# Kernel optimization log

Measured on AMD Instinct MI355X. Metric: run time of the kernel, lower is better.

Reference implementation:

```python
import jax, jax.numpy as jnp
import numpy as np

B, N, M, NF = 8, 512, 100, 42
DIMS = [NF, 256, 128, 64, 1]


def setup_inputs() -> dict:
    key = jax.random.key(0)
    ks = jax.random.split(key, 3 + len(DIMS) - 1)
    inp = {
        "image": jax.random.normal(ks[0], (B, N, NF), jnp.float32),
        "dfeat": jax.random.normal(ks[1], (B, N, M, NF, 3), jnp.float32) * 0.1,
        "neighbor": jax.random.randint(ks[2], (B, N, M), 0, N + 1),  # 0 = no neighbor, else 1-based atom idx
    }
    for l in range(len(DIMS) - 1):
        inp[f"W{l}"] = jax.random.normal(ks[3 + l], (DIMS[l], DIMS[l + 1]), jnp.float32) / np.sqrt(DIMS[l])
        inp[f"b{l}"] = jnp.zeros((DIMS[l + 1],), jnp.float32)
    return inp


def _atom_energy(x, Ws, bs):
    # per-atom MLP: sigmoid hidden layers, linear scalar output
    h = x
    for W, b in zip(Ws[:-1], bs[:-1]):
        h = jax.nn.sigmoid(h @ W + b)
    return (h @ Ws[-1] + bs[-1])[0]


def reference(image, dfeat, neighbor, W0, b0, W1, b1, W2, b2, W3, b3):
    Ws = (W0, W1, W2, W3)
    bs = (b0, b1, b2, b3)
    nb, na, nf = image.shape

    e_fn = lambda x: _atom_energy(x, Ws, bs)
    flat = image.reshape(-1, nf)
    Ei = jax.vmap(e_fn)(flat).reshape(nb, na)                      # [B, N]
    dE = jax.vmap(jax.grad(e_fn))(flat).reshape(nb, na, nf)        # dEi/dFeat, [B, N, F]
    Etot = jnp.sum(Ei, axis=1, keepdims=True)                      # [B, 1]

    # Force[b,i,:] = sum_m dE[b, neighbor[b,i,m]-1, :] @ dfeat[b,i,m,:,:], masking pad (0) entries
    mask = (neighbor > 0).astype(dE.dtype)                         # [B, N, M]
    idx = jnp.maximum(neighbor - 1, 0)                             # [B, N, M]
    dE_g = jax.vmap(lambda d, i: d[i])(dE, idx)                    # [B, N, M, F]
    Force = jnp.einsum('bnmf,bnmfd->bnd', dE_g * mask[..., None], dfeat)  # [B, N, 3]
    return Etot, Ei, Force
```

## Files before the change

kernel.cpp:

```cpp
#include <hip/hip_runtime.h>

#define NFEAT 42
#define H1 256
#define H2 128
#define H3 64
#define NB 8
#define NA 512
#define NM 100
#define TA 4

__device__ __forceinline__ float sigmoidf(float z) {
    return 1.0f / (1.0f + __expf(-z));
}

__global__ __launch_bounds__(256) void transpose_weights(
    const float* __restrict__ W0, const float* __restrict__ W1, const float* __restrict__ W2,
    float* __restrict__ W0T, float* __restrict__ W1T, float* __restrict__ W2T)
{
    int i = blockIdx.x * 256 + threadIdx.x;
    if (i < H1 * NFEAT) {
        int k = i / NFEAT, f = i - k * NFEAT;
        W0T[i] = W0[f * H1 + k];
    }
    if (i < H2 * H1) {
        int j = i >> 8, k = i & 255;
        W1T[i] = W1[k * H2 + j];
    }
    if (i < H3 * H2) {
        int k = i >> 7, j = i & 127;
        W2T[i] = W2[j * H3 + k];
    }
}

__global__ __launch_bounds__(256) void mlp_fwd_bwd(
    const float* __restrict__ image,
    const float* __restrict__ W0, const float* __restrict__ b0,
    const float* __restrict__ W1, const float* __restrict__ b1,
    const float* __restrict__ W2, const float* __restrict__ b2,
    const float* __restrict__ W3, const float* __restrict__ b3,
    const float* __restrict__ W0T, const float* __restrict__ W1T, const float* __restrict__ W2T,
    float* __restrict__ Ei,
    float* __restrict__ dE)
{
    const int t = threadIdx.x;
    const int atom0 = blockIdx.x * TA;

    __shared__ __align__(16) float sx[TA][NFEAT + 2];
    __shared__ __align__(16) float sh1[TA][H1];
    __shared__ __align__(16) float sh2[TA][H2];
    __shared__ __align__(16) float sh3[TA][H3];
    __shared__ __align__(16) float sd3[TA][H3];
    __shared__ __align__(16) float sd2[TA][H2];
    __shared__ __align__(16) float sd1[TA][H1];

    for (int i = t; i < TA * NFEAT; i += 256) {
        int a = i / NFEAT, f = i - a * NFEAT;
        sx[a][f] = image[(atom0 + a) * NFEAT + f];
    }
    __syncthreads();

    {
        float acc[TA] = {0.f, 0.f, 0.f, 0.f};
        for (int kk = 0; kk < 10; ++kk) {
            float w0_ = W0[(4 * kk + 0) * H1 + t];
            float w1_ = W0[(4 * kk + 1) * H1 + t];
            float w2_ = W0[(4 * kk + 2) * H1 + t];
            float w3_ = W0[(4 * kk + 3) * H1 + t];
            #pragma unroll
            for (int a = 0; a < TA; ++a) {
                float4 h = ((const float4*)sx[a])[kk];
                acc[a] += h.x * w0_ + h.y * w1_ + h.z * w2_ + h.w * w3_;
            }
        }
        float wa = W0[40 * H1 + t], wb = W0[41 * H1 + t];
        float bb = b0[t];
        #pragma unroll
        for (int a = 0; a < TA; ++a) {
            acc[a] += sx[a][40] * wa + sx[a][41] * wb;
            sh1[a][t] = sigmoidf(acc[a] + bb);
        }
    }
    __syncthreads();

    {
        const int j = t & 127, a0 = (t >> 7) * 2;
        float acc[2] = {0.f, 0.f};
        for (int kk = 0; kk < H1 / 4; ++kk) {
            float w0_ = W1[(4 * kk + 0) * H2 + j];
            float w1_ = W1[(4 * kk + 1) * H2 + j];
            float w2_ = W1[(4 * kk + 2) * H2 + j];
            float w3_ = W1[(4 * kk + 3) * H2 + j];
            #pragma unroll
            for (int a = 0; a < 2; ++a) {
                float4 h = ((const float4*)sh1[a0 + a])[kk];
                acc[a] += h.x * w0_ + h.y * w1_ + h.z * w2_ + h.w * w3_;
            }
        }
        float bb = b1[j];
        #pragma unroll
        for (int a = 0; a < 2; ++a) sh2[a0 + a][j] = sigmoidf(acc[a] + bb);
    }
    __syncthreads();

    {
        const int j = t & 63, a = t >> 6;
        float acc = 0.f;
        for (int kk = 0; kk < H2 / 4; ++kk) {
            float w0_ = W2[(4 * kk + 0) * H3 + j];
            float w1_ = W2[(4 * kk + 1) * H3 + j];
            float w2_ = W2[(4 * kk + 2) * H3 + j];
            float w3_ = W2[(4 * kk + 3) * H3 + j];
            float4 h = ((const float4*)sh2[a])[kk];
            acc += h.x * w0_ + h.y * w1_ + h.z * w2_ + h.w * w3_;
        }
        sh3[a][j] = sigmoidf(acc + b2[j]);
    }
    __syncthreads();

    {
        const int lane = t & 63, a = t >> 6;
        float w = W3[lane];
        float h = sh3[a][lane];
        sd3[a][lane] = w * h * (1.f - h);
        float v = w * h;
        #pragma unroll
        for (int off = 32; off > 0; off >>= 1) v += __shfl_down(v, off, 64);
        if (lane == 0) Ei[atom0 + a] = v + b3[0];
    }
    __syncthreads();

    {
        const int j = t & 127, a0 = (t >> 7) * 2;
        float acc[2] = {0.f, 0.f};
        for (int kk = 0; kk < H3 / 4; ++kk) {
            float w0_ = W2T[(4 * kk + 0) * H2 + j];
            float w1_ = W2T[(4 * kk + 1) * H2 + j];
            float w2_ = W2T[(4 * kk + 2) * H2 + j];
            float w3_ = W2T[(4 * kk + 3) * H2 + j];
            #pragma unroll
            for (int a = 0; a < 2; ++a) {
                float4 d = ((const float4*)sd3[a0 + a])[kk];
                acc[a] += d.x * w0_ + d.y * w1_ + d.z * w2_ + d.w * w3_;
            }
        }
        #pragma unroll
        for (int a = 0; a < 2; ++a) {
            float h = sh2[a0 + a][j];
            sd2[a0 + a][j] = acc[a] * h * (1.f - h);
        }
    }
    __syncthreads();

    {
        float acc[TA] = {0.f, 0.f, 0.f, 0.f};
        for (int jj = 0; jj < H2 / 4; ++jj) {
            float w0_ = W1T[(4 * jj + 0) * H1 + t];
            float w1_ = W1T[(4 * jj + 1) * H1 + t];
            float w2_ = W1T[(4 * jj + 2) * H1 + t];
            float w3_ = W1T[(4 * jj + 3) * H1 + t];
            #pragma unroll
            for (int a = 0; a < TA; ++a) {
                float4 d = ((const float4*)sd2[a])[jj];
                acc[a] += d.x * w0_ + d.y * w1_ + d.z * w2_ + d.w * w3_;
            }
        }
        #pragma unroll
        for (int a = 0; a < TA; ++a) {
            float h = sh1[a][t];
            sd1[a][t] = acc[a] * h * (1.f - h);
        }
    }
    __syncthreads();

    {
        const int f = t & 63, a = t >> 6;
        if (f < NFEAT) {
            float acc = 0.f;
            for (int kk = 0; kk < H1 / 4; ++kk) {
                float w0_ = W0T[(4 * kk + 0) * NFEAT + f];
                float w1_ = W0T[(4 * kk + 1) * NFEAT + f];
                float w2_ = W0T[(4 * kk + 2) * NFEAT + f];
                float w3_ = W0T[(4 * kk + 3) * NFEAT + f];
                float4 d = ((const float4*)sd1[a])[kk];
                acc += d.x * w0_ + d.y * w1_ + d.z * w2_ + d.w * w3_;
            }
            dE[(atom0 + a) * NFEAT + f] = acc;
        }
    }
}

__global__ __launch_bounds__(256) void etot_kernel(const float* __restrict__ Ei,
                                                   float* __restrict__ Etot)
{
    const int b = blockIdx.x;
    const int t = threadIdx.x;
    float v = Ei[b * NA + t] + Ei[b * NA + t + 256];
    __shared__ float red[4];
    #pragma unroll
    for (int off = 32; off > 0; off >>= 1) v += __shfl_down(v, off, 64);
    if ((t & 63) == 0) red[t >> 6] = v;
    __syncthreads();
    if (t == 0) Etot[b] = red[0] + red[1] + red[2] + red[3];
}

__global__ __launch_bounds__(256) void force_kernel(
    const float* __restrict__ dfeat,
    const int*   __restrict__ neighbor,
    const float* __restrict__ dE,
    float* __restrict__ Force)
{
    const int bi = blockIdx.x;
    const int b  = bi >> 9;
    const int t  = threadIdx.x;

    __shared__ int   s_nb[NM];
    __shared__ float s_dE[104 * NFEAT];
    __shared__ float s_part[1008];
    __shared__ float s_red[126];

    if (t < NM) s_nb[t] = neighbor[bi * NM + t];
    for (int i = t; i < 4 * NFEAT; i += 256) s_dE[NM * NFEAT + i] = 0.f;
    __syncthreads();

    for (int i = t; i < NM * NFEAT; i += 256) {
        int m = i / NFEAT, f = i - m * NFEAT;
        int n = s_nb[m];
        s_dE[i] = (n > 0) ? dE[((b << 9) + n - 1) * NFEAT + f] : 0.f;
    }
    __syncthreads();

    if (t < 252) {
        const int e4 = 4 * t;
        int off[4];
        #pragma unroll
        for (int c = 0; c < 4; ++c) {
            int ee = e4 + c;
            int r  = ee / 126;
            int e  = ee - r * 126;
            off[c] = r * NFEAT + e / 3;
        }
        const float* base = dfeat + (size_t)bi * (NM * NFEAT * 3);
        float acc[4] = {0.f, 0.f, 0.f, 0.f};

        for (int m0 = 0; m0 < 48; m0 += 8) {
            float4 vA = *(const float4*)(base + m0 * 126 + e4);
            float4 vB = *(const float4*)(base + (m0 + 48) * 126 + e4);
            const float* sdA = s_dE + m0 * NFEAT;
            const float* sdB = s_dE + (m0 + 48) * NFEAT;
            acc[0] += vA.x * sdA[off[0]] + vB.x * sdB[off[0]];
            acc[1] += vA.y * sdA[off[1]] + vB.y * sdB[off[1]];
            acc[2] += vA.z * sdA[off[2]] + vB.z * sdB[off[2]];
            acc[3] += vA.w * sdA[off[3]] + vB.w * sdB[off[3]];
        }
        {
            const int m0 = 96;
            float vv[4];
            if (bi != NB * NA - 1) {
                float4 v = *(const float4*)(base + m0 * 126 + e4);
                vv[0] = v.x; vv[1] = v.y; vv[2] = v.z; vv[3] = v.w;
            } else {
                #pragma unroll
                for (int c = 0; c < 4; ++c) {
                    int r = (e4 + c) / 126;
                    vv[c] = (m0 + r < NM) ? base[m0 * 126 + e4 + c] : 0.f;
                }
            }
            const float* sd = s_dE + m0 * NFEAT;
            #pragma unroll
            for (int c = 0; c < 4; ++c) acc[c] += vv[c] * sd[off[c]];
        }
        #pragma unroll
        for (int c = 0; c < 4; ++c) s_part[e4 + c] = acc[c];
    }
    __syncthreads();

    if (t < 126) {
        float s = 0.f;
        #pragma unroll
        for (int r = 0; r < 8; ++r) s += s_part[r * 126 + t];
        s_red[t] = s;
    }
    __syncthreads();

    if (t < 3) {
        float s = 0.f;
        #pragma unroll
        for (int f = 0; f < NFEAT; ++f) s += s_red[f * 3 + t];
        Force[bi * 3 + t] = s;
    }
}

extern "C" void kernel_launch(void* const* d_in, const int* in_sizes, int n_in,
                              void* d_out, int out_size, void* d_ws, size_t ws_size,
                              hipStream_t stream) {
    const float* image    = (const float*)d_in[0];
    const float* dfeat    = (const float*)d_in[1];
    const int*   neighbor = (const int*)  d_in[2];
    const float* W0 = (const float*)d_in[3];
    const float* b0 = (const float*)d_in[4];
    const float* W1 = (const float*)d_in[5];
    const float* b1 = (const float*)d_in[6];
    const float* W2 = (const float*)d_in[7];
    const float* b2 = (const float*)d_in[8];
    const float* W3 = (const float*)d_in[9];
    const float* b3 = (const float*)d_in[10];

    float* out   = (float*)d_out;
    float* Etot  = out;
    float* Ei    = out + NB;
    float* Force = out + NB + NB * NA;

    float* dE  = (float*)d_ws;
    float* W0T = dE  + NB * NA * NFEAT;
    float* W1T = W0T + H1 * NFEAT;
    float* W2T = W1T + H2 * H1;

    transpose_weights<<<(H1 * H2 + 255) / 256, 256, 0, stream>>>(W0, W1, W2, W0T, W1T, W2T);
    mlp_fwd_bwd<<<(NB * NA) / TA, 256, 0, stream>>>(image, W0, b0, W1, b1, W2, b2, W3, b3,
                                                    W0T, W1T, W2T, Ei, dE);
    etot_kernel<<<NB, 256, 0, stream>>>(Ei, Etot);
    force_kernel<<<NB * NA, 256, 0, stream>>>(dfeat, neighbor, dE, Force);
}
```

Baseline: 346.6 us.

## Stage MLP weights through shared memory and double atoms per block

```diff
diff --git a/kernel.cpp b/kernel.cpp
--- a/kernel.cpp
+++ b/kernel.cpp
@@ -7,7 +7,7 @@
 #define NB 8
 #define NA 512
 #define NM 100
-#define TA 4
+#define TA 8
 
 __device__ __forceinline__ float sigmoidf(float z) {
     return 1.0f / (1.0f + __expf(-z));
@@ -52,27 +52,52 @@
     __shared__ __align__(16) float sd3[TA][H3];
     __shared__ __align__(16) float sd2[TA][H2];
     __shared__ __align__(16) float sd1[TA][H1];
+    __shared__ __align__(16) float wbuf[6144];
+
+    auto stage = [&](const float* src, int nf) {
+        __syncthreads();
+        const float4* s4 = (const float4*)src;
+        float4* d4 = (float4*)wbuf;
+        int n4 = nf >> 2;
+        for (int i = t; i < n4; i += 256) d4[i] = s4[i];
+        __syncthreads();
+    };
 
     for (int i = t; i < TA * NFEAT; i += 256) {
         int a = i / NFEAT, f = i - a * NFEAT;
         sx[a][f] = image[(atom0 + a) * NFEAT + f];
     }
-    __syncthreads();
-
-    {
-        float acc[TA] = {0.f, 0.f, 0.f, 0.f};
-        for (int kk = 0; kk < 10; ++kk) {
-            float w0_ = W0[(4 * kk + 0) * H1 + t];
-            float w1_ = W0[(4 * kk + 1) * H1 + t];
-            float w2_ = W0[(4 * kk + 2) * H1 + t];
-            float w3_ = W0[(4 * kk + 3) * H1 + t];
+
+    {
+        float acc[TA];
+        #pragma unroll
+        for (int a = 0; a < TA; ++a) acc[a] = 0.f;
+
+        stage(W0, 24 * H1);
+        for (int kq = 0; kq < 6; ++kq) {
+            float w0_ = wbuf[(4 * kq + 0) * H1 + t];
+            float w1_ = wbuf[(4 * kq + 1) * H1 + t];
+            float w2_ = wbuf[(4 * kq + 2) * H1 + t];
+            float w3_ = wbuf[(4 * kq + 3) * H1 + t];
             #pragma unroll
             for (int a = 0; a < TA; ++a) {
-                float4 h = ((const float4*)sx[a])[kk];
+                float4 h = ((const float4*)sx[a])[kq];
                 acc[a] += h.x * w0_ + h.y * w1_ + h.z * w2_ + h.w * w3_;
             }
         }
-        float wa = W0[40 * H1 + t], wb = W0[41 * H1 + t];
+        stage(W0 + 24 * H1, 18 * H1);
+        for (int kq = 0; kq < 4; ++kq) {
+            float w0_ = wbuf[(4 * kq + 0) * H1 + t];
+            float w1_ = wbuf[(4 * kq + 1) * H1 + t];
+            float w2_ = wbuf[(4 * kq + 2) * H1 + t];
+            float w3_ = wbuf[(4 * kq + 3) * H1 + t];
+            #pragma unroll
+            for (int a = 0; a < TA; ++a) {
+                float4 h = ((const float4*)sx[a])[6 + kq];
+                acc[a] += h.x * w0_ + h.y * w1_ + h.z * w2_ + h.w * w3_;
+            }
+        }
+        float wa = wbuf[16 * H1 + t], wb = wbuf[17 * H1 + t];
         float bb = b0[t];
         #pragma unroll
         for (int a = 0; a < TA; ++a) {
@@ -80,88 +105,119 @@
             sh1[a][t] = sigmoidf(acc[a] + bb);
         }
     }
-    __syncthreads();
-
-    {
-        const int j = t & 127, a0 = (t >> 7) * 2;
+
+    {
+        const int j = t & 127, a0 = (t >> 7) * 4;
+        float acc[4] = {0.f, 0.f, 0.f, 0.f};
+        for (int c = 0; c < 6; ++c) {
+            const int k0 = 48 * c;
+            const int nrow = (c < 5) ? 48 : 16;
+            stage(W1 + k0 * H2, nrow * H2);
+            const int q0 = k0 >> 2;
+            for (int kq = 0; kq < nrow / 4; ++kq) {
+                float w0_ = wbuf[(4 * kq + 0) * H2 + j];
+                float w1_ = wbuf[(4 * kq + 1) * H2 + j];
+                float w2_ = wbuf[(4 * kq + 2) * H2 + j];
+                float w3_ = wbuf[(4 * kq + 3) * H2 + j];
+                #pragma unroll
+                for (int a = 0; a < 4; ++a) {
+                    float4 h = ((const float4*)sh1[a0 + a])[q0 + kq];
+                    acc[a] += h.x * w0_ + h.y * w1_ + h.z * w2_ + h.w * w3_;
+                }
+            }
+        }
+        float bb = b1[j];
+        #pragma unroll
+        for (int a = 0; a < 4; ++a) sh2[a0 + a][j] = sigmoidf(acc[a] + bb);
+    }
+
+    {
+        const int j = t & 63, a0 = (t >> 6) * 2;
         float acc[2] = {0.f, 0.f};
-        for (int kk = 0; kk < H1 / 4; ++kk) {
-            float w0_ = W1[(4 * kk + 0) * H2 + j];
-            float w1_ = W1[(4 * kk + 1) * H2 + j];
-            float w2_ = W1[(4 * kk + 2) * H2 + j];
-            float w3_ = W1[(4 * kk + 3) * H2 + j];
-            #pragma unroll
-            for (int a = 0; a < 2; ++a) {
-                float4 h = ((const float4*)sh1[a0 + a])[kk];
-                acc[a] += h.x * w0_ + h.y * w1_ + h.z * w2_ + h.w * w3_;
-            }
-        }
-        float bb = b1[j];
-        #pragma unroll
-        for (int a = 0; a < 2; ++a) sh2[a0 + a][j] = sigmoidf(acc[a] + bb);
-    }
-    __syncthreads();
-
-    {
-        const int j = t & 63, a = t >> 6;
-        float acc = 0.f;
-        for (int kk = 0; kk < H2 / 4; ++kk) {
-            float w0_ = W2[(4 * kk + 0) * H3 + j];
-            float w1_ = W2[(4 * kk + 1) * H3 + j];
-            float w2_ = W2[(4 * kk + 2) * H3 + j];
-            float w3_ = W2[(4 * kk + 3) * H3 + j];
-            float4 h = ((const float4*)sh2[a])[kk];
-            acc += h.x * w0_ + h.y * w1_ + h.z * w2_ + h.w * w3_;
-        }
-        sh3[a][j] = sigmoidf(acc + b2[j]);
-    }
-    __syncthreads();
-
-    {
-        const int lane = t & 63, a = t >> 6;
+        for (int c = 0; c < 2; ++c) {
+            const int k0 = (c == 0) ? 0 : 96;
+            const int nrow = (c == 0) ? 96 : 32;
+            stage(W2 + k0 * H3, nrow * H3);
+            const int q0 = k0 >> 2;
+            for (int kq = 0; kq < nrow / 4; ++kq) {
+                float w0_ = wbuf[(4 * kq + 0) * H3 + j];
+                float w1_ = wbuf[(4 * kq + 1) * H3 + j];
+                float w2_ = wbuf[(4 * kq + 2) * H3 + j];
+                float w3_ = wbuf[(4 * kq + 3) * H3 + j];
+                #pragma unroll
+                for (int a = 0; a < 2; ++a) {
+                    float4 h = ((const float4*)sh2[a0 + a])[q0 + kq];
+                    acc[a] += h.x * w0_ + h.y * w1_ + h.z * w2_ + h.w * w3_;
+                }
+            }
+        }
+        float bb = b2[j];
+        #pragma unroll
+        for (int a = 0; a < 2; ++a) sh3[a0 + a][j] = sigmoidf(acc[a] + bb);
+    }
+    __syncthreads();
+
+    {
+        const int lane = t & 63, a0 = (t >> 6) * 2;
         float w = W3[lane];
-        float h = sh3[a][lane];
-        sd3[a][lane] = w * h * (1.f - h);
-        float v = w * h;
-        #pragma unroll
-        for (int off = 32; off > 0; off >>= 1) v += __shfl_down(v, off, 64);
-        if (lane == 0) Ei[atom0 + a] = v + b3[0];
-    }
-    __syncthreads();
-
-    {
-        const int j = t & 127, a0 = (t >> 7) * 2;
-        float acc[2] = {0.f, 0.f};
-        for (int kk = 0; kk < H3 / 4; ++kk) {
-            float w0_ = W2T[(4 * kk + 0) * H2 + j];
-            float w1_ = W2T[(4 * kk + 1) * H2 + j];
-            float w2_ = W2T[(4 * kk + 2) * H2 + j];
-            float w3_ = W2T[(4 * kk + 3) * H2 + j];
-            #pragma unroll
-            for (int a = 0; a < 2; ++a) {
-                float4 d = ((const float4*)sd3[a0 + a])[kk];
-                acc[a] += d.x * w0_ + d.y * w1_ + d.z * w2_ + d.w * w3_;
-            }
-        }
-        #pragma unroll
-        for (int a = 0; a < 2; ++a) {
+        float bb = b3[0];
+        #pragma unroll
+        for (int a = a0; a < a0 + 2; ++a) {
+            float h = sh3[a][lane];
+            sd3[a][lane] = w * h * (1.f - h);
+            float v = w * h;
+            #pragma unroll
+            for (int off = 32; off > 0; off >>= 1) v += __shfl_down(v, off, 64);
+            if (lane == 0) Ei[atom0 + a] = v + bb;
+        }
+    }
+
+    {
+        const int j = t & 127, a0 = (t >> 7) * 4;
+        float acc[4] = {0.f, 0.f, 0.f, 0.f};
+        for (int c = 0; c < 2; ++c) {
+            const int k0 = (c == 0) ? 0 : 48;
+            const int nrow = (c == 0) ? 48 : 16;
+            stage(W2T + k0 * H2, nrow * H2);
+            const int q0 = k0 >> 2;
+            for (int kq = 0; kq < nrow / 4; ++kq) {
+                float w0_ = wbuf[(4 * kq + 0) * H2 + j];
+                float w1_ = wbuf[(4 * kq + 1) * H2 + j];
+                float w2_ = wbuf[(4 * kq + 2) * H2 + j];
+                float w3_ = wbuf[(4 * kq + 3) * H2 + j];
+                #pragma unroll
+                for (int a = 0; a < 4; ++a) {
+                    float4 d = ((const float4*)sd3[a0 + a])[q0 + kq];
+                    acc[a] += d.x * w0_ + d.y * w1_ + d.z * w2_ + d.w * w3_;
+                }
+            }
+        }
+        #pragma unroll
+        for (int a = 0; a < 4; ++a) {
             float h = sh2[a0 + a][j];
             sd2[a0 + a][j] = acc[a] * h * (1.f - h);
         }
     }
-    __syncthreads();
-
-    {
-        float acc[TA] = {0.f, 0.f, 0.f, 0.f};
-        for (int jj = 0; jj < H2 / 4; ++jj) {
-            float w0_ = W1T[(4 * jj + 0) * H1 + t];
-            float w1_ = W1T[(4 * jj + 1) * H1 + t];
-            float w2_ = W1T[(4 * jj + 2) * H1 + t];
-            float w3_ = W1T[(4 * jj + 3) * H1 + t];
-            #pragma unroll
-            for (int a = 0; a < TA; ++a) {
-                float4 d = ((const float4*)sd2[a])[jj];
-                acc[a] += d.x * w0_ + d.y * w1_ + d.z * w2_ + d.w * w3_;
+
+    {
+        float acc[TA];
+        #pragma unroll
+        for (int a = 0; a < TA; ++a) acc[a] = 0.f;
+        for (int c = 0; c < 6; ++c) {
+            const int j0 = 24 * c;
+            const int nrow = (c < 5) ? 24 : 8;
+            stage(W1T + j0 * H1, nrow * H1);
+            const int q0 = j0 >> 2;
+            for (int jq = 0; jq < nrow / 4; ++jq) {
+                float w0_ = wbuf[(4 * jq + 0) * H1 + t];
+                float w1_ = wbuf[(4 * jq + 1) * H1 + t];
+                float w2_ = wbuf[(4 * jq + 2) * H1 + t];
+                float w3_ = wbuf[(4 * jq + 3) * H1 + t];
+                #pragma unroll
+                for (int a = 0; a < TA; ++a) {
+                    float4 d = ((const float4*)sd2[a])[q0 + jq];
+                    acc[a] += d.x * w0_ + d.y * w1_ + d.z * w2_ + d.w * w3_;
+                }
             }
         }
         #pragma unroll
@@ -170,21 +226,33 @@
             sd1[a][t] = acc[a] * h * (1.f - h);
         }
     }
-    __syncthreads();
-
-    {
-        const int f = t & 63, a = t >> 6;
+
+    {
+        const int f = t & 63, a0 = (t >> 6) * 2;
+        float acc[2] = {0.f, 0.f};
+        for (int c = 0; c < 2; ++c) {
+            const int k0 = (c == 0) ? 0 : 144;
+            const int nrow = (c == 0) ? 144 : 112;
+            stage(W0T + k0 * NFEAT, nrow * NFEAT);
+            if (f < NFEAT) {
+                const int q0 = k0 >> 2;
+                for (int kq = 0; kq < nrow / 4; ++kq) {
+                    float w0_ = wbuf[(4 * kq + 0) * NFEAT + f];
+                    float w1_ = wbuf[(4 * kq + 1) * NFEAT + f];
+                    float w2_ = wbuf[(4 * kq + 2) * NFEAT + f];
+                    float w3_ = wbuf[(4 * kq + 3) * NFEAT + f];
+                    #pragma unroll
+                    for (int a = 0; a < 2; ++a) {
+                        float4 d = ((const float4*)sd1[a0 + a])[q0 + kq];
+                        acc[a] += d.x * w0_ + d.y * w1_ + d.z * w2_ + d.w * w3_;
+                    }
+                }
+            }
+        }
         if (f < NFEAT) {
-            float acc = 0.f;
-            for (int kk = 0; kk < H1 / 4; ++kk) {
-                float w0_ = W0T[(4 * kk + 0) * NFEAT + f];
-                float w1_ = W0T[(4 * kk + 1) * NFEAT + f];
-                float w2_ = W0T[(4 * kk + 2) * NFEAT + f];
-                float w3_ = W0T[(4 * kk + 3) * NFEAT + f];
-                float4 d = ((const float4*)sd1[a])[kk];
-                acc += d.x * w0_ + d.y * w1_ + d.z * w2_ + d.w * w3_;
-            }
-            dE[(atom0 + a) * NFEAT + f] = acc;
+            #pragma unroll
+            for (int a = 0; a < 2; ++a)
+                dE[(atom0 + a0 + a) * NFEAT + f] = acc[a];
         }
     }
 }
```

After: 638.9 us. 84.3% more time.

## Split fused per-atom MLP into layer-wise kernels with transposed activation layout

Applied to the files above, without the earlier changes.

```diff
diff --git a/kernel.cpp b/kernel.cpp
--- a/kernel.cpp
+++ b/kernel.cpp
@@ -7,10 +7,29 @@
 #define NB 8
 #define NA 512
 #define NM 100
-#define TA 4
+#define NTOT (NB * NA)
 
 __device__ __forceinline__ float sigmoidf(float z) {
     return 1.0f / (1.0f + __expf(-z));
+}
+
+template<int K, int JT>
+__device__ __forceinline__ void mv(const float* __restrict__ actT,
+                                   const float* __restrict__ WT,
+                                   int j0, int n, float* __restrict__ acc) {
+    static_assert(K % 64 == 0, "K must be a multiple of 64");
+    #pragma unroll
+    for (int c = 0; c < K / 64; ++c) {
+        float act[64];
+        #pragma unroll
+        for (int i = 0; i < 64; ++i) act[i] = actT[(c * 64 + i) * NTOT + n];
+        #pragma unroll
+        for (int j = 0; j < JT; ++j) {
+            const float* w = WT + (j0 + j) * K + c * 64;
+            #pragma unroll
+            for (int i = 0; i < 64; ++i) acc[j] += act[i] * w[i];
+        }
+    }
 }
 
 __global__ __launch_bounds__(256) void transpose_weights(
@@ -19,8 +38,8 @@
 {
     int i = blockIdx.x * 256 + threadIdx.x;
     if (i < H1 * NFEAT) {
-        int k = i / NFEAT, f = i - k * NFEAT;
-        W0T[i] = W0[f * H1 + k];
+        int j = i / NFEAT, f = i - j * NFEAT;
+        W0T[i] = W0[f * H1 + j];
     }
     if (i < H2 * H1) {
         int j = i >> 8, k = i & 255;
@@ -32,161 +51,125 @@
     }
 }
 
-__global__ __launch_bounds__(256) void mlp_fwd_bwd(
-    const float* __restrict__ image,
-    const float* __restrict__ W0, const float* __restrict__ b0,
-    const float* __restrict__ W1, const float* __restrict__ b1,
-    const float* __restrict__ W2, const float* __restrict__ b2,
-    const float* __restrict__ W3, const float* __restrict__ b3,
-    const float* __restrict__ W0T, const float* __restrict__ W1T, const float* __restrict__ W2T,
-    float* __restrict__ Ei,
+__global__ __launch_bounds__(256) void l0_fwd(
+    const float* __restrict__ image, const float* __restrict__ W0T,
+    const float* __restrict__ b0, float* __restrict__ h1T)
+{
+    const int t = threadIdx.x;
+    const int n0 = blockIdx.x * 256;
+    const int j0 = blockIdx.y * 8;
+
+    __shared__ float sx[256 * 43];
+    for (int i = t; i < 256 * NFEAT; i += 256) {
+        int n = i / NFEAT, f = i - n * NFEAT;
+        sx[n * 43 + f] = image[n0 * NFEAT + i];
+    }
+    __syncthreads();
+
+    float act[NFEAT];
+    #pragma unroll
+    for (int f = 0; f < NFEAT; ++f) act[f] = sx[t * 43 + f];
+
+    float acc[8];
+    #pragma unroll
+    for (int j = 0; j < 8; ++j) acc[j] = b0[j0 + j];
+    #pragma unroll
+    for (int j = 0; j < 8; ++j) {
+        const float* w = W0T + (j0 + j) * NFEAT;
+        #pragma unroll
+        for (int f = 0; f < NFEAT; ++f) acc[j] += act[f] * w[f];
+    }
+    const int n = n0 + t;
+    #pragma unroll
+    for (int j = 0; j < 8; ++j) h1T[(j0 + j) * NTOT + n] = sigmoidf(acc[j]);
+}
+
+__global__ __launch_bounds__(256) void l1_fwd(
+    const float* __restrict__ h1T, const float* __restrict__ W1T,
+    const float* __restrict__ b1, float* __restrict__ h2T)
+{
+    const int n = blockIdx.x * 256 + threadIdx.x;
+    const int j0 = blockIdx.y * 8;
+    float acc[8];
+    #pragma unroll
+    for (int j = 0; j < 8; ++j) acc[j] = b1[j0 + j];
+    mv<H1, 8>(h1T, W1T, j0, n, acc);
+    #pragma unroll
+    for (int j = 0; j < 8; ++j) h2T[(j0 + j) * NTOT + n] = sigmoidf(acc[j]);
+}
+
+__global__ __launch_bounds__(256) void l2_fwd(
+    const float* __restrict__ h2T, const float* __restrict__ W2T,
+    const float* __restrict__ b2, float* __restrict__ h3T)
+{
+    const int n = blockIdx.x * 256 + threadIdx.x;
+    const int j0 = blockIdx.y * 4;
+    float acc[4];
+    #pragma unroll
+    for (int j = 0; j < 4; ++j) acc[j] = b2[j0 + j];
+    mv<H2, 4>(h2T, W2T, j0, n, acc);
+    #pragma unroll
+    for (int j = 0; j < 4; ++j) h3T[(j0 + j) * NTOT + n] = sigmoidf(acc[j]);
+}
+
+__global__ __launch_bounds__(256) void l3_ei(
+    const float* __restrict__ h3T, const float* __restrict__ W3,
+    const float* __restrict__ b3, float* __restrict__ Ei, float* __restrict__ d3T)
+{
+    const int n = blockIdx.x * 256 + threadIdx.x;
+    float e = b3[0];
+    #pragma unroll
+    for (int k = 0; k < H3; ++k) {
+        float w = W3[k];
+        float h = h3T[k * NTOT + n];
+        e += w * h;
+        d3T[k * NTOT + n] = w * h * (1.f - h);
+    }
+    Ei[n] = e;
+}
+
+__global__ __launch_bounds__(256) void bwd_d2(
+    const float* __restrict__ d3T, const float* __restrict__ W2,
+    const float* __restrict__ h2T, float* __restrict__ d2T)
+{
+    const int n = blockIdx.x * 256 + threadIdx.x;
+    const int j0 = blockIdx.y * 4;
+    float acc[4] = {0.f, 0.f, 0.f, 0.f};
+    mv<H3, 4>(d3T, W2, j0, n, acc);
+    #pragma unroll
+    for (int j = 0; j < 4; ++j) {
+        float h = h2T[(j0 + j) * NTOT + n];
+        d2T[(j0 + j) * NTOT + n] = acc[j] * h * (1.f - h);
+    }
+}
+
+__global__ __launch_bounds__(256) void bwd_d1(
+    const float* __restrict__ d2T, const float* __restrict__ W1,
+    const float* __restrict__ h1T, float* __restrict__ d1T)
+{
+    const int n = blockIdx.x * 256 + threadIdx.x;
+    const int j0 = blockIdx.y * 8;
+    float acc[8] = {0.f, 0.f, 0.f, 0.f, 0.f, 0.f, 0.f, 0.f};
+    mv<H2, 8>(d2T, W1, j0, n, acc);
+    #pragma unroll
+    for (int j = 0; j < 8; ++j) {
+        float h = h1T[(j0 + j) * NTOT + n];
+        d1T[(j0 + j) * NTOT + n] = acc[j] * h * (1.f - h);
+    }
+}
+
+__global__ __launch_bounds__(256) void bwd_dE(
+    const float* __restrict__ d1T, const float* __restrict__ W0,
     float* __restrict__ dE)
 {
-    const int t = threadIdx.x;
-    const int atom0 = blockIdx.x * TA;
-
-    __shared__ __align__(16) float sx[TA][NFEAT + 2];
-    __shared__ __align__(16) float sh1[TA][H1];
-    __shared__ __align__(16) float sh2[TA][H2];
-    __shared__ __align__(16) float sh3[TA][H3];
-    __shared__ __align__(16) float sd3[TA][H3];
-    __shared__ __align__(16) float sd2[TA][H2];
-    __shared__ __align__(16) float sd1[TA][H1];
-
-    for (int i = t; i < TA * NFEAT; i += 256) {
-        int a = i / NFEAT, f = i - a * NFEAT;
-        sx[a][f] = image[(atom0 + a) * NFEAT + f];
-    }
-    __syncthreads();
-
-    {
-        float acc[TA] = {0.f, 0.f, 0.f, 0.f};
-        for (int kk = 0; kk < 10; ++kk) {
-            float w0_ = W0[(4 * kk + 0) * H1 + t];
-            float w1_ = W0[(4 * kk + 1) * H1 + t];
-            float w2_ = W0[(4 * kk + 2) * H1 + t];
-            float w3_ = W0[(4 * kk + 3) * H1 + t];
-            #pragma unroll
-            for (int a = 0; a < TA; ++a) {
-                float4 h = ((const float4*)sx[a])[kk];
-                acc[a] += h.x * w0_ + h.y * w1_ + h.z * w2_ + h.w * w3_;
-            }
-        }
-        float wa = W0[40 * H1 + t], wb = W0[41 * H1 + t];
-        float bb = b0[t];
-        #pragma unroll
-        for (int a = 0; a < TA; ++a) {
-            acc[a] += sx[a][40] * wa + sx[a][41] * wb;
-            sh1[a][t] = sigmoidf(acc[a] + bb);
-        }
-    }
-    __syncthreads();
-
-    {
-        const int j = t & 127, a0 = (t >> 7) * 2;
-        float acc[2] = {0.f, 0.f};
-        for (int kk = 0; kk < H1 / 4; ++kk) {
-            float w0_ = W1[(4 * kk + 0) * H2 + j];
-            float w1_ = W1[(4 * kk + 1) * H2 + j];
-            float w2_ = W1[(4 * kk + 2) * H2 + j];
-            float w3_ = W1[(4 * kk + 3) * H2 + j];
-            #pragma unroll
-            for (int a = 0; a < 2; ++a) {
-                float4 h = ((const float4*)sh1[a0 + a])[kk];
-                acc[a] += h.x * w0_ + h.y * w1_ + h.z * w2_ + h.w * w3_;
-            }
-        }
-        float bb = b1[j];
-        #pragma unroll
-        for (int a = 0; a < 2; ++a) sh2[a0 + a][j] = sigmoidf(acc[a] + bb);
-    }
-    __syncthreads();
-
-    {
-        const int j = t & 63, a = t >> 6;
-        float acc = 0.f;
-        for (int kk = 0; kk < H2 / 4; ++kk) {
-            float w0_ = W2[(4 * kk + 0) * H3 + j];
-            float w1_ = W2[(4 * kk + 1) * H3 + j];
-            float w2_ = W2[(4 * kk + 2) * H3 + j];
-            float w3_ = W2[(4 * kk + 3) * H3 + j];
-            float4 h = ((const float4*)sh2[a])[kk];
-            acc += h.x * w0_ + h.y * w1_ + h.z * w2_ + h.w * w3_;
-        }
-        sh3[a][j] = sigmoidf(acc + b2[j]);
-    }
-    __syncthreads();
-
-    {
-        const int lane = t & 63, a = t >> 6;
-        float w = W3[lane];
-        float h = sh3[a][lane];
-        sd3[a][lane] = w * h * (1.f - h);
-        float v = w * h;
-        #pragma unroll
-        for (int off = 32; off > 0; off >>= 1) v += __shfl_down(v, off, 64);
-        if (lane == 0) Ei[atom0 + a] = v + b3[0];
-    }
-    __syncthreads();
-
-    {
-        const int j = t & 127, a0 = (t >> 7) * 2;
-        float acc[2] = {0.f, 0.f};
-        for (int kk = 0; kk < H3 / 4; ++kk) {
-            float w0_ = W2T[(4 * kk + 0) * H2 + j];
-            float w1_ = W2T[(4 * kk + 1) * H2 + j];
-            float w2_ = W2T[(4 * kk + 2) * H2 + j];
-            float w3_ = W2T[(4 * kk + 3) * H2 + j];
-            #pragma unroll
-            for (int a = 0; a < 2; ++a) {
-                float4 d = ((const float4*)sd3[a0 + a])[kk];
-                acc[a] += d.x * w0_ + d.y * w1_ + d.z * w2_ + d.w * w3_;
-            }
-        }
-        #pragma unroll
-        for (int a = 0; a < 2; ++a) {
-            float h = sh2[a0 + a][j];
-            sd2[a0 + a][j] = acc[a] * h * (1.f - h);
-        }
-    }
-    __syncthreads();
-
-    {
-        float acc[TA] = {0.f, 0.f, 0.f, 0.f};
-        for (int jj = 0; jj < H2 / 4; ++jj) {
-            float w0_ = W1T[(4 * jj + 0) * H1 + t];
-            float w1_ = W1T[(4 * jj + 1) * H1 + t];
-            float w2_ = W1T[(4 * jj + 2) * H1 + t];
-            float w3_ = W1T[(4 * jj + 3) * H1 + t];
-            #pragma unroll
-            for (int a = 0; a < TA; ++a) {
-                float4 d = ((const float4*)sd2[a])[jj];
-                acc[a] += d.x * w0_ + d.y * w1_ + d.z * w2_ + d.w * w3_;
-            }
-        }
-        #pragma unroll
-        for (int a = 0; a < TA; ++a) {
-            float h = sh1[a][t];
-            sd1[a][t] = acc[a] * h * (1.f - h);
-        }
-    }
-    __syncthreads();
-
-    {
-        const int f = t & 63, a = t >> 6;
-        if (f < NFEAT) {
-            float acc = 0.f;
-            for (int kk = 0; kk < H1 / 4; ++kk) {
-                float w0_ = W0T[(4 * kk + 0) * NFEAT + f];
-                float w1_ = W0T[(4 * kk + 1) * NFEAT + f];
-                float w2_ = W0T[(4 * kk + 2) * NFEAT + f];
-                float w3_ = W0T[(4 * kk + 3) * NFEAT + f];
-                float4 d = ((const float4*)sd1[a])[kk];
-                acc += d.x * w0_ + d.y * w1_ + d.z * w2_ + d.w * w3_;
-            }
-            dE[(atom0 + a) * NFEAT + f] = acc;
-        }
-    }
+    const int n = blockIdx.x * 256 + threadIdx.x;
+    const int f0 = blockIdx.y * 14;
+    float acc[14];
+    #pragma unroll
+    for (int j = 0; j < 14; ++j) acc[j] = 0.f;
+    mv<H1, 14>(d1T, W0, f0, n, acc);
+    #pragma unroll
+    for (int j = 0; j < 14; ++j) dE[n * NFEAT + f0 + j] = acc[j];
 }
 
 __global__ __launch_bounds__(256) void etot_kernel(const float* __restrict__ Ei,
@@ -255,7 +238,7 @@
         {
             const int m0 = 96;
             float vv[4];
-            if (bi != NB * NA - 1) {
+            if (bi != NTOT - 1) {
                 float4 v = *(const float4*)(base + m0 * 126 + e4);
                 vv[0] = v.x; vv[1] = v.y; vv[2] = v.z; vv[3] = v.w;
             } else {
@@ -308,16 +291,28 @@
     float* out   = (float*)d_out;
     float* Etot  = out;
     float* Ei    = out + NB;
-    float* Force = out + NB + NB * NA;
-
-    float* dE  = (float*)d_ws;
-    float* W0T = dE  + NB * NA * NFEAT;
-    float* W1T = W0T + H1 * NFEAT;
-    float* W2T = W1T + H2 * H1;
+    float* Force = out + NB + NTOT;
+
+    float* p   = (float*)d_ws;
+    float* dE  = p;  p += NTOT * NFEAT;
+    float* W0T = p;  p += H1 * NFEAT;
+    float* W1T = p;  p += H2 * H1;
+    float* W2T = p;  p += H3 * H2;
+    float* h1T = p;  p += H1 * NTOT;
+    float* h2T = p;  p += H2 * NTOT;
+    float* h3T = p;  p += H3 * NTOT;
+    float* d3T = p;  p += H3 * NTOT;
+    float* d2T = p;  p += H2 * NTOT;
+    float* d1T = p;  p += H1 * NTOT;
 
     transpose_weights<<<(H1 * H2 + 255) / 256, 256, 0, stream>>>(W0, W1, W2, W0T, W1T, W2T);
-    mlp_fwd_bwd<<<(NB * NA) / TA, 256, 0, stream>>>(image, W0, b0, W1, b1, W2, b2, W3, b3,
-                                                    W0T, W1T, W2T, Ei, dE);
-    etot_kernel<<<NB, 256, 0, stream>>>(Ei, Etot);
-    force_kernel<<<NB * NA, 256, 0, stream>>>(dfeat, neighbor, dE, Force);
-}
+    l0_fwd <<<dim3(16, 32), 256, 0, stream>>>(image, W0T, b0, h1T);
+    l1_fwd <<<dim3(16, 16), 256, 0, stream>>>(h1T, W1T, b1, h2T);
+    l2_fwd <<<dim3(16, 16), 256, 0, stream>>>(h2T, W2T, b2, h3T);
+    l3_ei  <<<16, 256, 0, stream>>>(h3T, W3, b3, Ei, d3T);
+    bwd_d2 <<<dim3(16, 32), 256, 0, stream>>>(d3T, W2, h2T, d2T);
+    bwd_d1 <<<dim3(16, 32), 256, 0, stream>>>(d2T, W1, h1T, d1T);
+    bwd_dE <<<dim3(16, 3),  256, 0, stream>>>(d1T, W0, dE);
+    etot_kernel <<<NB, 256, 0, stream>>>(Ei, Etot);
+    force_kernel<<<NTOT, 256, 0, stream>>>(dfeat, neighbor, dE, Force);
+}
```

Result: slower. 423.2 us (+22.1%).

## Retile MLP kernel to 8 atoms per block with float4 weight loads; batch dfeat loads

Applied to the files above, without the earlier changes.

```diff
diff --git a/kernel.cpp b/kernel.cpp
--- a/kernel.cpp
+++ b/kernel.cpp
@@ -7,7 +7,8 @@
 #define NB 8
 #define NA 512
 #define NM 100
-#define TA 4
+#define NTOT (NB * NA)
+#define TA 8
 
 __device__ __forceinline__ float sigmoidf(float z) {
     return 1.0f / (1.0f + __expf(-z));
@@ -39,8 +40,7 @@
     const float* __restrict__ W2, const float* __restrict__ b2,
     const float* __restrict__ W3, const float* __restrict__ b3,
     const float* __restrict__ W0T, const float* __restrict__ W1T, const float* __restrict__ W2T,
-    float* __restrict__ Ei,
-    float* __restrict__ dE)
+    float* __restrict__ Ei, float* __restrict__ dE)
 {
     const int t = threadIdx.x;
     const int atom0 = blockIdx.x * TA;
@@ -60,131 +60,124 @@
     __syncthreads();
 
     {
-        float acc[TA] = {0.f, 0.f, 0.f, 0.f};
-        for (int kk = 0; kk < 10; ++kk) {
-            float w0_ = W0[(4 * kk + 0) * H1 + t];
-            float w1_ = W0[(4 * kk + 1) * H1 + t];
-            float w2_ = W0[(4 * kk + 2) * H1 + t];
-            float w3_ = W0[(4 * kk + 3) * H1 + t];
+        const int jj = t & 63, g = t >> 6;
+        const int a0 = 2 * g, a1 = 2 * g + 1;
+        float4 acc0 = {0.f, 0.f, 0.f, 0.f}, acc1 = {0.f, 0.f, 0.f, 0.f};
+        for (int k = 0; k < NFEAT; ++k) {
+            float4 w = *(const float4*)&W0[k * H1 + 4 * jj];
+            float x0 = sx[a0][k], x1 = sx[a1][k];
+            acc0.x += x0 * w.x; acc0.y += x0 * w.y; acc0.z += x0 * w.z; acc0.w += x0 * w.w;
+            acc1.x += x1 * w.x; acc1.y += x1 * w.y; acc1.z += x1 * w.z; acc1.w += x1 * w.w;
+        }
+        float4 bb = *(const float4*)&b0[4 * jj];
+        float4 o0 = {sigmoidf(acc0.x + bb.x), sigmoidf(acc0.y + bb.y),
+                     sigmoidf(acc0.z + bb.z), sigmoidf(acc0.w + bb.w)};
+        float4 o1 = {sigmoidf(acc1.x + bb.x), sigmoidf(acc1.y + bb.y),
+                     sigmoidf(acc1.z + bb.z), sigmoidf(acc1.w + bb.w)};
+        *(float4*)&sh1[a0][4 * jj] = o0;
+        *(float4*)&sh1[a1][4 * jj] = o1;
+    }
+    __syncthreads();
+
+    {
+        const int jj = t & 31, a = t >> 5;
+        float4 acc = {0.f, 0.f, 0.f, 0.f};
+        #pragma unroll 4
+        for (int k = 0; k < H1; ++k) {
+            float4 w = *(const float4*)&W1[k * H2 + 4 * jj];
+            float h = sh1[a][k];
+            acc.x += h * w.x; acc.y += h * w.y; acc.z += h * w.z; acc.w += h * w.w;
+        }
+        float4 bb = *(const float4*)&b1[4 * jj];
+        float4 o = {sigmoidf(acc.x + bb.x), sigmoidf(acc.y + bb.y),
+                    sigmoidf(acc.z + bb.z), sigmoidf(acc.w + bb.w)};
+        *(float4*)&sh2[a][4 * jj] = o;
+    }
+    __syncthreads();
+
+    if (t < 128) {
+        const int jj = t & 15, a = t >> 4;
+        float4 acc = {0.f, 0.f, 0.f, 0.f};
+        #pragma unroll 4
+        for (int k = 0; k < H2; ++k) {
+            float4 w = *(const float4*)&W2[k * H3 + 4 * jj];
+            float h = sh2[a][k];
+            acc.x += h * w.x; acc.y += h * w.y; acc.z += h * w.z; acc.w += h * w.w;
+        }
+        float4 bb = *(const float4*)&b2[4 * jj];
+        float4 o = {sigmoidf(acc.x + bb.x), sigmoidf(acc.y + bb.y),
+                    sigmoidf(acc.z + bb.z), sigmoidf(acc.w + bb.w)};
+        *(float4*)&sh3[a][4 * jj] = o;
+    }
+    __syncthreads();
+
+    {
+        const int lane = t & 63, a0 = (t >> 6) * 2;
+        float w = W3[lane];
+        float bb = b3[0];
+        #pragma unroll
+        for (int a = a0; a < a0 + 2; ++a) {
+            float h = sh3[a][lane];
+            sd3[a][lane] = w * h * (1.f - h);
+            float v = w * h;
             #pragma unroll
-            for (int a = 0; a < TA; ++a) {
-                float4 h = ((const float4*)sx[a])[kk];
-                acc[a] += h.x * w0_ + h.y * w1_ + h.z * w2_ + h.w * w3_;
+            for (int off = 32; off > 0; off >>= 1) v += __shfl_down(v, off, 64);
+            if (lane == 0) Ei[atom0 + a] = v + bb;
+        }
+    }
+    __syncthreads();
+
+    {
+        const int jj = t & 31, a = t >> 5;
+        float4 acc = {0.f, 0.f, 0.f, 0.f};
+        #pragma unroll 4
+        for (int k = 0; k < H3; ++k) {
+            float4 w = *(const float4*)&W2T[k * H2 + 4 * jj];
+            float d = sd3[a][k];
+            acc.x += d * w.x; acc.y += d * w.y; acc.z += d * w.z; acc.w += d * w.w;
+        }
+        float4 h = *(const float4*)&sh2[a][4 * jj];
+        float4 o = {acc.x * h.x * (1.f - h.x), acc.y * h.y * (1.f - h.y),
+                    acc.z * h.z * (1.f - h.z), acc.w * h.w * (1.f - h.w)};
+        *(float4*)&sd2[a][4 * jj] = o;
+    }
+    __syncthreads();
+
+    {
+        const int kk = t & 63, g = t >> 6;
+        const int a0 = 2 * g, a1 = 2 * g + 1;
+        float4 acc0 = {0.f, 0.f, 0.f, 0.f}, acc1 = {0.f, 0.f, 0.f, 0.f};
+        #pragma unroll 4
+        for (int j = 0; j < H2; ++j) {
+            float4 w = *(const float4*)&W1T[j * H1 + 4 * kk];
+            float d0 = sd2[a0][j], d1v = sd2[a1][j];
+            acc0.x += d0 * w.x; acc0.y += d0 * w.y; acc0.z += d0 * w.z; acc0.w += d0 * w.w;
+            acc1.x += d1v * w.x; acc1.y += d1v * w.y; acc1.z += d1v * w.z; acc1.w += d1v * w.w;
+        }
+        float4 h0 = *(const float4*)&sh1[a0][4 * kk];
+        float4 h1v = *(const float4*)&sh1[a1][4 * kk];
+        float4 o0 = {acc0.x * h0.x * (1.f - h0.x), acc0.y * h0.y * (1.f - h0.y),
+                     acc0.z * h0.z * (1.f - h0.z), acc0.w * h0.w * (1.f - h0.w)};
+        float4 o1 = {acc1.x * h1v.x * (1.f - h1v.x), acc1.y * h1v.y * (1.f - h1v.y),
+                     acc1.z * h1v.z * (1.f - h1v.z), acc1.w * h1v.w * (1.f - h1v.w)};
+        *(float4*)&sd1[a0][4 * kk] = o0;
+        *(float4*)&sd1[a1][4 * kk] = o1;
+    }
+    __syncthreads();
+
+    {
+        const int f = t & 63, g = t >> 6;
+        if (f < NFEAT) {
+            const int a0 = 2 * g, a1 = 2 * g + 1;
+            float acc0 = 0.f, acc1 = 0.f;
+            #pragma unroll 4
+            for (int k = 0; k < H1; ++k) {
+                float w = W0T[k * NFEAT + f];
+                acc0 += sd1[a0][k] * w;
+                acc1 += sd1[a1][k] * w;
             }
-        }
-        float wa = W0[40 * H1 + t], wb = W0[41 * H1 + t];
-        float bb = b0[t];
-        #pragma unroll
-        for (int a = 0; a < TA; ++a) {
-            acc[a] += sx[a][40] * wa + sx[a][41] * wb;
-            sh1[a][t] = sigmoidf(acc[a] + bb);
-        }
-    }
-    __syncthreads();
-
-    {
-        const int j = t & 127, a0 = (t >> 7) * 2;
-        float acc[2] = {0.f, 0.f};
-        for (int kk = 0; kk < H1 / 4; ++kk) {
-            float w0_ = W1[(4 * kk + 0) * H2 + j];
-            float w1_ = W1[(4 * kk + 1) * H2 + j];
-            float w2_ = W1[(4 * kk + 2) * H2 + j];
-            float w3_ = W1[(4 * kk + 3) * H2 + j];
-            #pragma unroll
-            for (int a = 0; a < 2; ++a) {
-                float4 h = ((const float4*)sh1[a0 + a])[kk];
-                acc[a] += h.x * w0_ + h.y * w1_ + h.z * w2_ + h.w * w3_;
-            }
-        }
-        float bb = b1[j];
-        #pragma unroll
-        for (int a = 0; a < 2; ++a) sh2[a0 + a][j] = sigmoidf(acc[a] + bb);
-    }
-    __syncthreads();
-
-    {
-        const int j = t & 63, a = t >> 6;
-        float acc = 0.f;
-        for (int kk = 0; kk < H2 / 4; ++kk) {
-            float w0_ = W2[(4 * kk + 0) * H3 + j];
-            float w1_ = W2[(4 * kk + 1) * H3 + j];
-            float w2_ = W2[(4 * kk + 2) * H3 + j];
-            float w3_ = W2[(4 * kk + 3) * H3 + j];
-            float4 h = ((const float4*)sh2[a])[kk];
-            acc += h.x * w0_ + h.y * w1_ + h.z * w2_ + h.w * w3_;
-        }
-        sh3[a][j] = sigmoidf(acc + b2[j]);
-    }
-    __syncthreads();
-
-    {
-        const int lane = t & 63, a = t >> 6;
-        float w = W3[lane];
-        float h = sh3[a][lane];
-        sd3[a][lane] = w * h * (1.f - h);
-        float v = w * h;
-        #pragma unroll
-        for (int off = 32; off > 0; off >>= 1) v += __shfl_down(v, off, 64);
-        if (lane == 0) Ei[atom0 + a] = v + b3[0];
-    }
-    __syncthreads();
-
-    {
-        const int j = t & 127, a0 = (t >> 7) * 2;
-        float acc[2] = {0.f, 0.f};
-        for (int kk = 0; kk < H3 / 4; ++kk) {
-            float w0_ = W2T[(4 * kk + 0) * H2 + j];
-            float w1_ = W2T[(4 * kk + 1) * H2 + j];
-            float w2_ = W2T[(4 * kk + 2) * H2 + j];
-            float w3_ = W2T[(4 * kk + 3) * H2 + j];
-            #pragma unroll
-            for (int a = 0; a < 2; ++a) {
-                float4 d = ((const float4*)sd3[a0 + a])[kk];
-                acc[a] += d.x * w0_ + d.y * w1_ + d.z * w2_ + d.w * w3_;
-            }
-        }
-        #pragma unroll
-        for (int a = 0; a < 2; ++a) {
-            float h = sh2[a0 + a][j];
-            sd2[a0 + a][j] = acc[a] * h * (1.f - h);
-        }
-    }
-    __syncthreads();
-
-    {
-        float acc[TA] = {0.f, 0.f, 0.f, 0.f};
-        for (int jj = 0; jj < H2 / 4; ++jj) {
-            float w0_ = W1T[(4 * jj + 0) * H1 + t];
-            float w1_ = W1T[(4 * jj + 1) * H1 + t];
-            float w2_ = W1T[(4 * jj + 2) * H1 + t];
-            float w3_ = W1T[(4 * jj + 3) * H1 + t];
-            #pragma unroll
-            for (int a = 0; a < TA; ++a) {
-                float4 d = ((const float4*)sd2[a])[jj];
-                acc[a] += d.x * w0_ + d.y * w1_ + d.z * w2_ + d.w * w3_;
-            }
-        }
-        #pragma unroll
-        for (int a = 0; a < TA; ++a) {
-            float h = sh1[a][t];
-            sd1[a][t] = acc[a] * h * (1.f - h);
-        }
-    }
-    __syncthreads();
-
-    {
-        const int f = t & 63, a = t >> 6;
-        if (f < NFEAT) {
-            float acc = 0.f;
-            for (int kk = 0; kk < H1 / 4; ++kk) {
-                float w0_ = W0T[(4 * kk + 0) * NFEAT + f];
-                float w1_ = W0T[(4 * kk + 1) * NFEAT + f];
-                float w2_ = W0T[(4 * kk + 2) * NFEAT + f];
-                float w3_ = W0T[(4 * kk + 3) * NFEAT + f];
-                float4 d = ((const float4*)sd1[a])[kk];
-                acc += d.x * w0_ + d.y * w1_ + d.z * w2_ + d.w * w3_;
-            }
-            dE[(atom0 + a) * NFEAT + f] = acc;
+            dE[(atom0 + a0) * NFEAT + f] = acc0;
+            dE[(atom0 + a1) * NFEAT + f] = acc1;
         }
     }
 }
@@ -242,22 +235,27 @@
         const float* base = dfeat + (size_t)bi * (NM * NFEAT * 3);
         float acc[4] = {0.f, 0.f, 0.f, 0.f};
 
-        for (int m0 = 0; m0 < 48; m0 += 8) {
-            float4 vA = *(const float4*)(base + m0 * 126 + e4);
-            float4 vB = *(const float4*)(base + (m0 + 48) * 126 + e4);
-            const float* sdA = s_dE + m0 * NFEAT;
-            const float* sdB = s_dE + (m0 + 48) * NFEAT;
-            acc[0] += vA.x * sdA[off[0]] + vB.x * sdB[off[0]];
-            acc[1] += vA.y * sdA[off[1]] + vB.y * sdB[off[1]];
-            acc[2] += vA.z * sdA[off[2]] + vB.z * sdB[off[2]];
-            acc[3] += vA.w * sdA[off[3]] + vB.w * sdB[off[3]];
+        float4 v[12];
+        #pragma unroll
+        for (int u = 0; u < 6; ++u) {
+            v[2 * u]     = *(const float4*)(base + (u * 8) * 126 + e4);
+            v[2 * u + 1] = *(const float4*)(base + (u * 8 + 48) * 126 + e4);
+        }
+        #pragma unroll
+        for (int u = 0; u < 6; ++u) {
+            const float* sdA = s_dE + (u * 8) * NFEAT;
+            const float* sdB = s_dE + (u * 8 + 48) * NFEAT;
+            acc[0] += v[2 * u].x * sdA[off[0]] + v[2 * u + 1].x * sdB[off[0]];
+            acc[1] += v[2 * u].y * sdA[off[1]] + v[2 * u + 1].y * sdB[off[1]];
+            acc[2] += v[2 * u].z * sdA[off[2]] + v[2 * u + 1].z * sdB[off[2]];
+            acc[3] += v[2 * u].w * sdA[off[3]] + v[2 * u + 1].w * sdB[off[3]];
         }
         {
             const int m0 = 96;
             float vv[4];
-            if (bi != NB * NA - 1) {
-                float4 v = *(const float4*)(base + m0 * 126 + e4);
-                vv[0] = v.x; vv[1] = v.y; vv[2] = v.z; vv[3] = v.w;
+            if (bi != NTOT - 1) {
+                float4 w = *(const float4*)(base + m0 * 126 + e4);
+                vv[0] = w.x; vv[1] = w.y; vv[2] = w.z; vv[3] = w.w;
             } else {
                 #pragma unroll
                 for (int c = 0; c < 4; ++c) {
@@ -308,16 +306,16 @@
     float* out   = (float*)d_out;
     float* Etot  = out;
     float* Ei    = out + NB;
-    float* Force = out + NB + NB * NA;
+    float* Force = out + NB + NTOT;
 
     float* dE  = (float*)d_ws;
-    float* W0T = dE  + NB * NA * NFEAT;
+    float* W0T = dE  + NTOT * NFEAT;
     float* W1T = W0T + H1 * NFEAT;
     float* W2T = W1T + H2 * H1;
 
     transpose_weights<<<(H1 * H2 + 255) / 256, 256, 0, stream>>>(W0, W1, W2, W0T, W1T, W2T);
-    mlp_fwd_bwd<<<(NB * NA) / TA, 256, 0, stream>>>(image, W0, b0, W1, b1, W2, b2, W3, b3,
-                                                    W0T, W1T, W2T, Ei, dE);
+    mlp_fwd_bwd<<<NTOT / TA, 256, 0, stream>>>(image, W0, b0, W1, b1, W2, b2, W3, b3,
+                                               W0T, W1T, W2T, Ei, dE);
     etot_kernel<<<NB, 256, 0, stream>>>(Ei, Etot);
-    force_kernel<<<NB * NA, 256, 0, stream>>>(dfeat, neighbor, dE, Force);
-}
+    force_kernel<<<NTOT, 256, 0, stream>>>(dfeat, neighbor, dE, Force);
+}
```

New measurement: 366.7 us. +5.8%, slower.
